# Optimization experiments

Measured on AMD Instinct MI355X. Metric: run time of the kernel, lower is better.

The kernel has to match this reference:

```python
import jax, jax.numpy as jnp
import numpy as np

N, C, L, K = 8, 128, 1024, 100   # batch, channels, encoded seq len, num_negatives
TEMP = 0.5                        # contrastive temperature
EPS = 1e-8                        # cosine-similarity norm clamp (torch default)


def setup_inputs() -> dict:
    key = jax.random.key(0)
    kz, kc, kn = jax.random.split(key, 3)
    z = jax.random.normal(kz, (N, C, L), dtype=jnp.float32)
    c = jax.random.normal(kc, (N, C, L + 1), dtype=jnp.float32)
    # Uniform sampling of K distinct indices per (n, l), excluding l itself:
    # equivalent to torch.multinomial(ones(L,L)-eye(L), K) per row, per sample.
    noise = jax.random.uniform(kn, (N, L, L), dtype=jnp.float32)
    noise = noise - 2.0 * jnp.eye(L, dtype=jnp.float32)  # push self-index below everything
    _, neg_inds = jax.lax.top_k(noise, K)                # (N, L, K) int32, distinct, != l
    return {"z": z, "c": c, "neg_inds": neg_inds.astype(jnp.int32)}


def reference(z, c, neg_inds):
    # z: (N, C, L) unmasked convencoder features; c: (N, C, L+1) transformer out
    n, ch, l = z.shape
    z_seq = jnp.transpose(z, (0, 2, 1))                  # (N, L, C)
    # gather negatives: (N, L, K, C)
    negatives = z_seq[jnp.arange(n)[:, None, None], neg_inds]
    # drop start token, move to (N, L, 1, C)
    c_seq = jnp.transpose(c[..., 1:], (0, 2, 1))[:, :, None, :]
    z_tgt = z_seq[:, :, None, :]                         # (N, L, 1, C)
    targets = jnp.concatenate([z_tgt, negatives], axis=2)  # (N, L, K+1, C)
    # cosine similarity along C with torch-style eps clamping
    dot = jnp.sum(c_seq * targets, axis=-1)              # (N, L, K+1)
    c_norm = jnp.maximum(jnp.sqrt(jnp.sum(c_seq * c_seq, axis=-1)), EPS)
    t_norm = jnp.maximum(jnp.sqrt(jnp.sum(targets * targets, axis=-1)), EPS)
    logits = dot / (c_norm * t_norm) / TEMP              # (N, L, K+1)
    # mask negatives that exactly equal the context vector
    neg_in_tgt = jnp.all(c_seq == negatives, axis=-1)    # (N, L, K)
    neg_logits = jnp.where(neg_in_tgt, -jnp.inf, logits[:, :, 1:])
    logits = jnp.concatenate([logits[:, :, :1], neg_logits], axis=2)
    return logits.reshape(-1, K + 1)                     # (N*L, K+1)
```

## Files before the change

kernel.cpp:

```cpp
#include <hip/hip_runtime.h>
#include <math.h>

#define N 8
#define C 128
#define L 1024
#define K 100
#define TEMP 0.5f
#define EPS 1e-8f
#define NT (N * L)

typedef _Float16 h2 __attribute__((ext_vector_type(2)));
union U4 { uint4 u; h2 h[4]; };

__device__ __forceinline__ float fd2(h2 a, h2 b, float acc) {
#if __has_builtin(__builtin_amdgcn_fdot2)
    return __builtin_amdgcn_fdot2(a, b, acc, false);
#else
    return acc + (float)a[0] * (float)b[0] + (float)a[1] * (float)b[1];
#endif
}

#if __has_builtin(__builtin_amdgcn_mov_dpp)
#define DPP_ADD(x, ctrl) ((x) + __int_as_float(__builtin_amdgcn_mov_dpp(__float_as_int(x), (ctrl), 0xF, 0xF, true)))
#else
#define DPP_ADD(x, ctrl) ((x) + __shfl_xor((x), ((ctrl) == 0xB1 ? 1 : 2)))
#endif

__global__ void __launch_bounds__(512)
transpose_both(const float* __restrict__ z, const float* __restrict__ c,
               _Float16* __restrict__ z_h, _Float16* __restrict__ c_h,
               float* __restrict__ zp, float* __restrict__ cp) {
    __shared__ float tile[64][65];
    __shared__ float part[8][64];
    const int which = blockIdx.z >> 3;
    const int n = blockIdx.z & 7;
    const float* src = which ? c : z;
    _Float16* dst = which ? c_h : z_h;
    float* pdst = which ? cp : zp;
    const int slen = which ? (L + 1) : L;
    const int off = which;
    const int l0 = blockIdx.x * 64;
    const int c0 = blockIdx.y * 64;
    const int tx = threadIdx.x;
    const int ty = threadIdx.y;
#pragma unroll
    for (int i = 0; i < 8; i++) {
        int chn = c0 + ty + i * 8;
        tile[ty + i * 8][tx] = src[((size_t)(n * C + chn)) * slen + off + l0 + tx];
    }
    __syncthreads();
#pragma unroll
    for (int i = 0; i < 8; i++) {
        int l = l0 + ty + i * 8;
        dst[((size_t)n * L + l) * C + c0 + tx] = (_Float16)tile[tx][ty + i * 8];
    }
    float p = 0.f;
#pragma unroll
    for (int i = 0; i < 8; i++) { float v = tile[ty * 8 + i][tx]; p += v * v; }
    part[ty][tx] = p;
    __syncthreads();
    if (ty == 0) {
        float sm = 0.f;
#pragma unroll
        for (int i = 0; i < 8; i++) sm += part[i][tx];
        pdst[(((size_t)n << 10) + l0 + tx) * 2 + (c0 >> 6)] = sm;
    }
}

__global__ void __launch_bounds__(256)
ssl_main(const _Float16* __restrict__ zh, const _Float16* __restrict__ chh,
         const int* __restrict__ neg_inds,
         const float* __restrict__ zp, const float* __restrict__ cp,
         const float* __restrict__ z_orig, const float* __restrict__ c_orig,
         float* __restrict__ out) {
    const int tid  = threadIdx.x;
    const int lane = tid & 63;
    const int g    = lane >> 2;
    const int s    = lane & 3;
    const int nt   = blockIdx.x * 4 + (tid >> 6);
    const int n    = nt >> 10;
    const int t    = nt & (L - 1);

    const uint4* crow = (const uint4*)(chh + (size_t)nt * C);
    U4 cf[4];
#pragma unroll
    for (int j = 0; j < 4; j++) cf[j].u = crow[s + 4 * j];

    const float2 cpv = ((const float2*)cp)[nt];
    const float cn = cpv.x + cpv.y;
    const float rs_c = 2.0f * rsqrtf(fmaxf(cn, EPS * EPS));

    const int* ni = neg_inds + (size_t)nt * K;
    const _Float16* zbase = zh + (((size_t)n) << 10) * C;
    const float2* zp2 = (const float2*)zp + ((size_t)n << 10);

    int idxs[7];
#pragma unroll
    for (int i = 0; i < 7; i++) {
        int kk = i * 16 + g;
        idxs[i] = (kk == 0) ? t : ((kk <= K) ? ni[kk - 1] : 0);
    }
    float tns[7];
#pragma unroll
    for (int i = 0; i < 7; i++) { float2 tv = zp2[idxs[i]]; tns[i] = tv.x + tv.y; }

    U4 rows[7][4];
#pragma unroll
    for (int p = 0; p < 2; p++) {
        const uint4* zr = (const uint4*)(zbase + (size_t)idxs[p] * C);
#pragma unroll
        for (int j = 0; j < 4; j++) rows[p][j].u = zr[s + 4 * j];
    }

#pragma unroll
    for (int i = 0; i < 7; i++) {
        if (i + 2 < 7) {
            const uint4* zr = (const uint4*)(zbase + (size_t)idxs[i + 2] * C);
#pragma unroll
            for (int j = 0; j < 4; j++) rows[i + 2][j].u = zr[s + 4 * j];
        }

        float d0 = 0.f, d1 = 0.f;
#pragma unroll
        for (int j = 0; j < 4; j++) {
            d0 = fd2(cf[j].h[0], rows[i][j].h[0], d0);
            d1 = fd2(cf[j].h[1], rows[i][j].h[1], d1);
            d0 = fd2(cf[j].h[2], rows[i][j].h[2], d0);
            d1 = fd2(cf[j].h[3], rows[i][j].h[3], d1);
        }
        float dot = d0 + d1;
        dot = DPP_ADD(dot, 0xB1);
        dot = DPP_ADD(dot, 0x4E);

        int kk = i * 16 + g;
        if (s == 0 && kk <= K) {
            float logit = dot * rs_c * rsqrtf(fmaxf(tns[i], EPS * EPS));
            if (kk > 0) {
                float ds = cn - 2.f * dot + tns[i];
                if (ds < 0.05f * cn) {
                    bool eq = true;
                    for (int q = 0; q < C; q++) {
                        float cv = c_orig[((size_t)(n * C + q)) * (L + 1) + t + 1];
                        float zv = z_orig[((size_t)(n * C + q)) * L + idxs[i]];
                        eq = eq && (cv == zv);
                    }
                    if (eq) logit = -INFINITY;
                }
            }
            out[(size_t)nt * (K + 1) + kk] = logit;
        }
    }
}

extern "C" void kernel_launch(void* const* d_in, const int* in_sizes, int n_in,
                              void* d_out, int out_size, void* d_ws, size_t ws_size,
                              hipStream_t stream) {
    const float* z   = (const float*)d_in[0];
    const float* c   = (const float*)d_in[1];
    const int*   neg = (const int*)d_in[2];
    float* out = (float*)d_out;

    _Float16* z_h = (_Float16*)d_ws;
    _Float16* c_h = z_h + (size_t)NT * C;
    float* zp = (float*)(c_h + (size_t)NT * C);
    float* cp = zp + (size_t)NT * 2;

    transpose_both<<<dim3(L / 64, C / 64, 16), dim3(64, 8), 0, stream>>>(z, c, z_h, c_h, zp, cp);
    ssl_main<<<dim3(NT / 4), 256, 0, stream>>>(z_h, c_h, neg, zp, cp, z, c, out);
}
```

Measured before the change: 79.94 us.

## Replace per-negative gathered dot products with dense MFMA GEMM plus LDS gather

Each block computes dot products of 16 context rows against all 1024 z rows of the batch using f16 MFMA instructions, stores them in shared memory, then gathers the needed target/negative entries by index. This replaces scattered per-negative row loads and fdot2 reductions with contiguous loads and matrix-core math. In exchange it does roughly ten times more multiply-adds than needed, rereads the whole batch slice of z per block, and uses 64KB of LDS per block, which limits occupancy.

```diff
diff --git a/kernel.cpp b/kernel.cpp
--- a/kernel.cpp
+++ b/kernel.cpp
@@ -8,23 +8,10 @@
 #define TEMP 0.5f
 #define EPS 1e-8f
 #define NT (N * L)
+#define ROWS 16
 
-typedef _Float16 h2 __attribute__((ext_vector_type(2)));
-union U4 { uint4 u; h2 h[4]; };
-
-__device__ __forceinline__ float fd2(h2 a, h2 b, float acc) {
-#if __has_builtin(__builtin_amdgcn_fdot2)
-    return __builtin_amdgcn_fdot2(a, b, acc, false);
-#else
-    return acc + (float)a[0] * (float)b[0] + (float)a[1] * (float)b[1];
-#endif
-}
-
-#if __has_builtin(__builtin_amdgcn_mov_dpp)
-#define DPP_ADD(x, ctrl) ((x) + __int_as_float(__builtin_amdgcn_mov_dpp(__float_as_int(x), (ctrl), 0xF, 0xF, true)))
-#else
-#define DPP_ADD(x, ctrl) ((x) + __shfl_xor((x), ((ctrl) == 0xB1 ? 1 : 2)))
-#endif
+typedef _Float16 half8 __attribute__((ext_vector_type(8)));
+typedef float f32x4 __attribute__((ext_vector_type(4)));
 
 __global__ void __launch_bounds__(512)
 transpose_both(const float* __restrict__ z, const float* __restrict__ c,
@@ -67,88 +54,85 @@
     }
 }
 
-__global__ void __launch_bounds__(256)
-ssl_main(const _Float16* __restrict__ zh, const _Float16* __restrict__ chh,
-         const int* __restrict__ neg_inds,
-         const float* __restrict__ zp, const float* __restrict__ cp,
-         const float* __restrict__ z_orig, const float* __restrict__ c_orig,
-         float* __restrict__ out) {
+__global__ void __launch_bounds__(512)
+gemm_gather(const _Float16* __restrict__ zh, const _Float16* __restrict__ ch,
+            const int* __restrict__ neg_inds,
+            const float* __restrict__ zp, const float* __restrict__ cp,
+            const float* __restrict__ z_orig, const float* __restrict__ c_orig,
+            float* __restrict__ out) {
+    __shared__ float dotL[ROWS * L];
     const int tid  = threadIdx.x;
     const int lane = tid & 63;
-    const int g    = lane >> 2;
-    const int s    = lane & 3;
-    const int nt   = blockIdx.x * 4 + (tid >> 6);
-    const int n    = nt >> 10;
-    const int t    = nt & (L - 1);
+    const int w    = tid >> 6;
+    const int n    = blockIdx.x >> 6;
+    const int t0   = (blockIdx.x & 63) * ROWS;
 
-    const uint4* crow = (const uint4*)(chh + (size_t)nt * C);
-    U4 cf[4];
+    const int r16 = lane & 15;
+    const int kg  = lane >> 4;
+
+    const _Float16* Abase = ch + ((size_t)(n * L + t0)) * C;
+    const _Float16* Bbase = zh + ((size_t)(n * L)) * C;
+
+    half8 a[4];
 #pragma unroll
-    for (int j = 0; j < 4; j++) cf[j].u = crow[s + 4 * j];
+    for (int ks = 0; ks < 4; ks++)
+        a[ks] = *(const half8*)(Abase + (size_t)r16 * C + ks * 32 + kg * 8);
 
-    const float2 cpv = ((const float2*)cp)[nt];
-    const float cn = cpv.x + cpv.y;
-    const float rs_c = 2.0f * rsqrtf(fmaxf(cn, EPS * EPS));
+    f32x4 acc[8];
+#pragma unroll
+    for (int i = 0; i < 8; i++)
+#pragma unroll
+        for (int r = 0; r < 4; r++) acc[i][r] = 0.f;
 
-    const int* ni = neg_inds + (size_t)nt * K;
-    const _Float16* zbase = zh + (((size_t)n) << 10) * C;
-    const float2* zp2 = (const float2*)zp + ((size_t)n << 10);
-
-    int idxs[7];
+    const int c0w = w << 7;
 #pragma unroll
-    for (int i = 0; i < 7; i++) {
-        int kk = i * 16 + g;
-        idxs[i] = (kk == 0) ? t : ((kk <= K) ? ni[kk - 1] : 0);
-    }
-    float tns[7];
+    for (int ks = 0; ks < 4; ks++) {
 #pragma unroll
-    for (int i = 0; i < 7; i++) { float2 tv = zp2[idxs[i]]; tns[i] = tv.x + tv.y; }
-
-    U4 rows[7][4];
-#pragma unroll
-    for (int p = 0; p < 2; p++) {
-        const uint4* zr = (const uint4*)(zbase + (size_t)idxs[p] * C);
-#pragma unroll
-        for (int j = 0; j < 4; j++) rows[p][j].u = zr[s + 4 * j];
+        for (int nt = 0; nt < 8; nt++) {
+            const half8 b = *(const half8*)(Bbase
+                + (size_t)(c0w + nt * 16 + r16) * C + ks * 32 + kg * 8);
+            acc[nt] = __builtin_amdgcn_mfma_f32_16x16x32_f16(a[ks], b, acc[nt], 0, 0, 0);
+        }
     }
 
 #pragma unroll
-    for (int i = 0; i < 7; i++) {
-        if (i + 2 < 7) {
-            const uint4* zr = (const uint4*)(zbase + (size_t)idxs[i + 2] * C);
+    for (int nt = 0; nt < 8; nt++)
 #pragma unroll
-            for (int j = 0; j < 4; j++) rows[i + 2][j].u = zr[s + 4 * j];
+        for (int r = 0; r < 4; r++)
+            dotL[(kg * 4 + r) * L + c0w + nt * 16 + r16] = acc[nt][r];
+
+    __syncthreads();
+
+    const int row = tid >> 5;
+    const int sub = tid & 31;
+    const int t   = t0 + row;
+    const int ntg = (n << 10) + t;
+    const float2 cpv = ((const float2*)cp)[ntg];
+    const float cn = cpv.x + cpv.y;
+    const float rs_c = 2.0f * rsqrtf(fmaxf(cn, EPS * EPS));
+    const int* ni = neg_inds + (size_t)ntg * K;
+    const float2* zp2 = (const float2*)zp + ((size_t)n << 10);
+    float* orow = out + (size_t)ntg * (K + 1);
+
+    for (int kk = sub; kk <= K; kk += 32) {
+        const int col = (kk == 0) ? t : ni[kk - 1];
+        const float dot = dotL[row * L + col];
+        const float2 tv = zp2[col];
+        const float tn = tv.x + tv.y;
+        float logit = dot * rs_c * rsqrtf(fmaxf(tn, EPS * EPS));
+        if (kk > 0) {
+            const float ds = cn - 2.f * dot + tn;
+            if (ds < 0.05f * cn) {
+                bool eq = true;
+                for (int q = 0; q < C; q++) {
+                    float cv = c_orig[((size_t)(n * C + q)) * (L + 1) + t + 1];
+                    float zv = z_orig[((size_t)(n * C + q)) * L + col];
+                    eq = eq && (cv == zv);
+                }
+                if (eq) logit = -INFINITY;
+            }
         }
-
-        float d0 = 0.f, d1 = 0.f;
-#pragma unroll
-        for (int j = 0; j < 4; j++) {
-            d0 = fd2(cf[j].h[0], rows[i][j].h[0], d0);
-            d1 = fd2(cf[j].h[1], rows[i][j].h[1], d1);
-            d0 = fd2(cf[j].h[2], rows[i][j].h[2], d0);
-            d1 = fd2(cf[j].h[3], rows[i][j].h[3], d1);
-        }
-        float dot = d0 + d1;
-        dot = DPP_ADD(dot, 0xB1);
-        dot = DPP_ADD(dot, 0x4E);
-
-        int kk = i * 16 + g;
-        if (s == 0 && kk <= K) {
-            float logit = dot * rs_c * rsqrtf(fmaxf(tns[i], EPS * EPS));
-            if (kk > 0) {
-                float ds = cn - 2.f * dot + tns[i];
-                if (ds < 0.05f * cn) {
-                    bool eq = true;
-                    for (int q = 0; q < C; q++) {
-                        float cv = c_orig[((size_t)(n * C + q)) * (L + 1) + t + 1];
-                        float zv = z_orig[((size_t)(n * C + q)) * L + idxs[i]];
-                        eq = eq && (cv == zv);
-                    }
-                    if (eq) logit = -INFINITY;
-                }
-            }
-            out[(size_t)nt * (K + 1) + kk] = logit;
-        }
+        orow[kk] = logit;
     }
 }
 
@@ -166,5 +150,5 @@
     float* cp = zp + (size_t)NT * 2;
 
     transpose_both<<<dim3(L / 64, C / 64, 16), dim3(64, 8), 0, stream>>>(z, c, z_h, c_h, zp, cp);
-    ssl_main<<<dim3(NT / 4), 256, 0, stream>>>(z_h, c_h, neg, zp, cp, z, c, out);
+    gemm_gather<<<dim3(N * (L / ROWS)), 512, 0, stream>>>(z_h, c_h, neg, zp, cp, z, c, out);
 }
```

Result: slower. 86.79 us (+8.6%).
